# Performance work log

Hardware: AMD Instinct MI355X
Metric: run time of the kernel (lower is better)

## Reference

```python
import jax, jax.numpy as jnp
import numpy as np

T, H, I, E, K = 4096, 2048, 2816, 8, 2


def setup_inputs() -> dict:
    key = jax.random.key(0)
    k1, k2, k3, k4, k5 = jax.random.split(key, 5)
    x = jax.random.normal(k1, (T, H), dtype=jnp.float32)
    w13 = jax.random.normal(k2, (E, 2 * I, H), dtype=jnp.float32) * 0.02
    w2 = jax.random.normal(k3, (E, H, I), dtype=jnp.float32) * 0.02
    topk_weights = jax.random.uniform(k4, (T, K), dtype=jnp.float32)
    topk_ids = jax.random.randint(k5, (T, K), 0, E, dtype=jnp.int64)
    return {"x": x, "w13": w13, "w2": w2, "topk_weights": topk_weights, "topk_ids": topk_ids}


def reference(x, w13, w2, topk_weights, topk_ids):
    # SwiGLU MoE: per expert e, y_e = silu(x @ w1g_e^T) * (x @ w1u_e^T) @ w2_e^T
    # then combine with routing weights for the top-k selected experts.
    w_gate = w13[:, :I, :]   # [E, I, H]
    w_up = w13[:, I:, :]     # [E, I, H]
    gate = jnp.einsum('th,eih->eti', x, w_gate)  # [E, T, I]
    up = jnp.einsum('th,eih->eti', x, w_up)      # [E, T, I]
    act = jax.nn.silu(gate) * up                 # [E, T, I]
    y = jnp.einsum('eti,ehi->eth', act, w2)      # [E, T, H]
    # combine[t, e] = sum_k topk_weights[t, k] * (topk_ids[t, k] == e)
    onehot = (topk_ids[:, :, None] == jnp.arange(E)[None, None, :]).astype(x.dtype)  # [T, K, E]
    combine = jnp.einsum('tk,tke->te', topk_weights, onehot)  # [T, E]
    out = jnp.einsum('eth,te->th', y, combine)   # [T, H]
    return out
```

## Files before the change

### kernel.cpp

```cpp
#include <hip/hip_runtime.h>
#include <hip/hip_bf16.h>

#define TT 4096
#define HH 2048
#define CI 2816
#define EE 8
#define KK 2
#define TKN (TT * KK)
#define TM 128
#define BK 64
#define MAX_MT (TKN / TM + EE)
#define ROWS_PAD (MAX_MT * TM)

typedef short short8 __attribute__((ext_vector_type(8)));
typedef float floatx4 __attribute__((ext_vector_type(4)));

__device__ __forceinline__ unsigned short f2bf(float f) {
  unsigned u = __float_as_uint(f);
  return (unsigned short)((u + 0x8000u) >> 16);
}

__device__ __forceinline__ void cvt_store8(unsigned short* dst, float4 a, float4 b) {
  short8 v;
  v[0] = (short)f2bf(a.x); v[1] = (short)f2bf(a.y);
  v[2] = (short)f2bf(a.z); v[3] = (short)f2bf(a.w);
  v[4] = (short)f2bf(b.x); v[5] = (short)f2bf(b.y);
  v[6] = (short)f2bf(b.z); v[7] = (short)f2bf(b.w);
  *(short8*)dst = v;
}

__device__ __forceinline__ void gload_lds16(const unsigned short* g, unsigned short* l) {
  __builtin_amdgcn_global_load_lds(
      (const __attribute__((address_space(1))) unsigned int*)g,
      (__attribute__((address_space(3))) unsigned int*)l, 16, 0, 0);
}

__global__ void cvt_kernel(const float* __restrict__ src, unsigned short* __restrict__ dst,
                           int n8) {
  for (int i = blockIdx.x * blockDim.x + threadIdx.x; i < n8; i += gridDim.x * blockDim.x) {
    float4 a = ((const float4*)src)[2 * i];
    float4 b = ((const float4*)src)[2 * i + 1];
    cvt_store8(dst + (size_t)i * 8, a, b);
  }
}

__global__ void bucket_kernel(const int* __restrict__ ids, const float* __restrict__ tw,
                              int* __restrict__ hdr, int* __restrict__ tok,
                              float* __restrict__ wt) {
  __shared__ int cnt[EE];
  __shared__ int cur[EE];
  int tid = threadIdx.x;
  if (tid < EE) cnt[tid] = 0;
  __syncthreads();
  for (int p = tid; p < TKN; p += 256) atomicAdd(&cnt[ids[p]], 1);
  for (int r = tid; r < ROWS_PAD; r += 256) { tok[r] = 0; wt[r] = 0.f; }
  __syncthreads();
  if (tid == 0) {
    int rb = 0, tb = 0;
    for (int e = 0; e < EE; e++) {
      cur[e] = rb;
      int nt = (cnt[e] + TM - 1) / TM;
      for (int j = 0; j < nt; j++) hdr[1 + tb + j] = e;
      rb += nt * TM;
      tb += nt;
    }
    for (int m = tb; m < MAX_MT; m++) hdr[1 + m] = 0;
    hdr[0] = tb;
  }
  __syncthreads();
  for (int p = tid; p < TKN; p += 256) {
    int e = ids[p];
    int slot = atomicAdd(&cur[e], 1);
    tok[slot] = p / KK;
    wt[slot] = tw[p];
  }
}

__global__ __launch_bounds__(256, 2)
void gemm1_kernel(const unsigned short* __restrict__ xb, const unsigned short* __restrict__ w13b,
                  const int* __restrict__ hdr, const int* __restrict__ tok,
                  unsigned short* __restrict__ act) {
  const int mt = blockIdx.x;
  if (mt >= hdr[0]) return;
  const int e = hdr[1 + mt];
  const int bn = blockIdx.y;
  const int row_base = mt * TM;
  const int tid = threadIdx.x;
  const int lane = tid & 63;
  const int wave = tid >> 6;

  __shared__ __align__(16) unsigned short As[TM][BK];
  __shared__ __align__(16) unsigned short Bs[TM][BK];

  const int kcol = (lane & 7) * 8;
  const unsigned short* gA[4];
  const unsigned short* gB[4];
  unsigned short* lA[4];
  unsigned short* lB[4];
#pragma unroll
  for (int j = 0; j < 4; j++) {
    int r = wave * 32 + j * 8 + (lane >> 3);
    gA[j] = xb + (size_t)tok[row_base + r] * HH + kcol;
    int wrow = (r < 64) ? (bn * 64 + r) : (CI + bn * 64 + (r - 64));
    gB[j] = w13b + ((size_t)e * (2 * CI) + wrow) * HH + kcol;
    lA[j] = &As[wave * 32 + j * 8][0];
    lB[j] = &Bs[wave * 32 + j * 8][0];
  }

  floatx4 acc[2][8];
#pragma unroll
  for (int mi = 0; mi < 2; mi++)
#pragma unroll
    for (int ni = 0; ni < 8; ni++) acc[mi][ni] = (floatx4){0.f, 0.f, 0.f, 0.f};

  const int lrow = lane & 15;
  const int quad = lane >> 4;
  const int m0 = wave * 32;

  for (int k0 = 0; k0 < HH; k0 += BK) {
    __syncthreads();
#pragma unroll
    for (int j = 0; j < 4; j++) {
      gload_lds16(gA[j] + k0, lA[j]);
      gload_lds16(gB[j] + k0, lB[j]);
    }
    __syncthreads();
#pragma unroll
    for (int kh = 0; kh < 2; kh++) {
      short8 af0 = *(const short8*)&As[m0 + lrow][kh * 32 + quad * 8];
      short8 af1 = *(const short8*)&As[m0 + 16 + lrow][kh * 32 + quad * 8];
#pragma unroll
      for (int ni = 0; ni < 8; ni++) {
        short8 bf = *(const short8*)&Bs[ni * 16 + lrow][kh * 32 + quad * 8];
        acc[0][ni] = __builtin_amdgcn_mfma_f32_16x16x32_bf16(af0, bf, acc[0][ni], 0, 0, 0);
        acc[1][ni] = __builtin_amdgcn_mfma_f32_16x16x32_bf16(af1, bf, acc[1][ni], 0, 0, 0);
      }
    }
  }

  const int col0 = bn * 64;
#pragma unroll
  for (int mi = 0; mi < 2; mi++) {
#pragma unroll
    for (int ni = 0; ni < 4; ni++) {
#pragma unroll
      for (int r = 0; r < 4; r++) {
        float g = acc[mi][ni][r];
        float uu = acc[mi][ni + 4][r];
        float s = g / (1.f + __expf(-g));
        int row = row_base + m0 + mi * 16 + quad * 4 + r;
        int col = col0 + ni * 16 + lrow;
        act[(size_t)row * CI + col] = f2bf(s * uu);
      }
    }
  }
}

__global__ __launch_bounds__(256, 2)
void gemm2_kernel(const unsigned short* __restrict__ act, const unsigned short* __restrict__ w2b,
                  const int* __restrict__ hdr, const int* __restrict__ tok,
                  const float* __restrict__ wt, float* __restrict__ out) {
  const int mt = blockIdx.x;
  if (mt >= hdr[0]) return;
  const int e = hdr[1 + mt];
  const int h0 = blockIdx.y * TM;
  const int row_base = mt * TM;
  const int tid = threadIdx.x;
  const int lane = tid & 63;
  const int wave = tid >> 6;

  __shared__ __align__(16) unsigned short As[TM][BK];
  __shared__ __align__(16) unsigned short Bs[TM][BK];
  __shared__ int tok_s[TM];
  __shared__ float wt_s[TM];

  if (tid < TM) {
    tok_s[tid] = tok[row_base + tid];
    wt_s[tid] = wt[row_base + tid];
  }

  const int kcol = (lane & 7) * 8;
  const unsigned short* gA[4];
  const unsigned short* gB[4];
  unsigned short* lA[4];
  unsigned short* lB[4];
#pragma unroll
  for (int j = 0; j < 4; j++) {
    int r = wave * 32 + j * 8 + (lane >> 3);
    gA[j] = act + (size_t)(row_base + r) * CI + kcol;
    gB[j] = w2b + ((size_t)e * HH + h0 + r) * CI + kcol;
    lA[j] = &As[wave * 32 + j * 8][0];
    lB[j] = &Bs[wave * 32 + j * 8][0];
  }

  floatx4 acc[2][8];
#pragma unroll
  for (int mi = 0; mi < 2; mi++)
#pragma unroll
    for (int ni = 0; ni < 8; ni++) acc[mi][ni] = (floatx4){0.f, 0.f, 0.f, 0.f};

  const int lrow = lane & 15;
  const int quad = lane >> 4;
  const int m0 = wave * 32;

  for (int k0 = 0; k0 < CI; k0 += BK) {
    __syncthreads();
#pragma unroll
    for (int j = 0; j < 4; j++) {
      gload_lds16(gA[j] + k0, lA[j]);
      gload_lds16(gB[j] + k0, lB[j]);
    }
    __syncthreads();
#pragma unroll
    for (int kh = 0; kh < 2; kh++) {
      short8 af0 = *(const short8*)&As[m0 + lrow][kh * 32 + quad * 8];
      short8 af1 = *(const short8*)&As[m0 + 16 + lrow][kh * 32 + quad * 8];
#pragma unroll
      for (int ni = 0; ni < 8; ni++) {
        short8 bf = *(const short8*)&Bs[ni * 16 + lrow][kh * 32 + quad * 8];
        acc[0][ni] = __builtin_amdgcn_mfma_f32_16x16x32_bf16(af0, bf, acc[0][ni], 0, 0, 0);
        acc[1][ni] = __builtin_amdgcn_mfma_f32_16x16x32_bf16(af1, bf, acc[1][ni], 0, 0, 0);
      }
    }
  }

#pragma unroll
  for (int mi = 0; mi < 2; mi++) {
#pragma unroll
    for (int ni = 0; ni < 8; ni++) {
#pragma unroll
      for (int r = 0; r < 4; r++) {
        int lr = m0 + mi * 16 + quad * 4 + r;
        float w = wt_s[lr];
        if (w != 0.f) {
          atomicAdd(out + (size_t)tok_s[lr] * HH + h0 + ni * 16 + lrow, acc[mi][ni][r] * w);
        }
      }
    }
  }
}

extern "C" void kernel_launch(void* const* d_in, const int* in_sizes, int n_in,
                              void* d_out, int out_size, void* d_ws, size_t ws_size,
                              hipStream_t stream) {
  const float* x   = (const float*)d_in[0];
  const float* w13 = (const float*)d_in[1];
  const float* w2  = (const float*)d_in[2];
  const float* tw  = (const float*)d_in[3];
  const int*   ids = (const int*)d_in[4];
  float* out = (float*)d_out;

  char* ws = (char*)d_ws;
  int* hdr = (int*)ws;
  int* tok = (int*)(ws + 512);
  float* wt = (float*)(ws + 512 + ROWS_PAD * 4);
  unsigned short* act  = (unsigned short*)(ws + 74240);
  unsigned short* xb   = (unsigned short*)(ws + 74240 + 51904512ull);
  unsigned short* w13b = (unsigned short*)(ws + 74240 + 51904512ull + 16777216ull);
  unsigned short* w2b  = (unsigned short*)(ws + 74240 + 51904512ull + 16777216ull + 184549376ull);

  hipMemsetAsync(d_out, 0, (size_t)out_size * sizeof(float), stream);
  bucket_kernel<<<1, 256, 0, stream>>>(ids, tw, hdr, tok, wt);
  cvt_kernel<<<2048, 256, 0, stream>>>(x, xb, TT * HH / 8);
  cvt_kernel<<<4096, 256, 0, stream>>>(w13, w13b, EE * 2 * CI * HH / 8);
  cvt_kernel<<<4096, 256, 0, stream>>>(w2, w2b, EE * HH * CI / 8);
  gemm1_kernel<<<dim3(MAX_MT, CI / 64), 256, 0, stream>>>(xb, w13b, hdr, tok, act);
  gemm2_kernel<<<dim3(MAX_MT, HH / TM), 256, 0, stream>>>(act, w2b, hdr, tok, wt, out);
}
```

Before: 1.189 ms.

## Use 2x2 wave tiling and XOR-swizzled LDS layout in MoE GEMMs

Both grouped GEMM kernels switch from a 4x1 wave layout (32 rows x 128 cols per wave) to a 2x2 layout (64x64 per wave), which cuts LDS fragment reads per MFMA from 10 loads per 16 MFMAs to 8. The LDS tiles are XOR-swizzled on the 16-byte chunk index, both in the global-to-LDS load and in the fragment reads, to avoid bank conflicts on the 128-byte row stride. Launch bounds are raised to 4 blocks per CU, which limits register use and risks spills given the 64-register accumulator.

New measurement: 1.524 ms. 28.2% more time.

```diff
diff --git a/kernel.cpp b/kernel.cpp
--- a/kernel.cpp
+++ b/kernel.cpp
@@ -33,6 +33,10 @@
   __builtin_amdgcn_global_load_lds(
       (const __attribute__((address_space(1))) unsigned int*)g,
       (__attribute__((address_space(3))) unsigned int*)l, 16, 0, 0);
+}
+
+__device__ __forceinline__ short8 lds_frag(const unsigned short (*tile)[BK], int row, int chunk) {
+  return *(const short8*)&tile[row][((chunk ^ (row & 7)) << 3)];
 }
 
 __global__ void cvt_kernel(const float* __restrict__ src, unsigned short* __restrict__ dst,
@@ -76,7 +80,7 @@
   }
 }
 
-__global__ __launch_bounds__(256, 2)
+__global__ __launch_bounds__(256, 4)
 void gemm1_kernel(const unsigned short* __restrict__ xb, const unsigned short* __restrict__ w13b,
                   const int* __restrict__ hdr, const int* __restrict__ tok,
                   unsigned short* __restrict__ act) {
@@ -88,11 +92,13 @@
   const int tid = threadIdx.x;
   const int lane = tid & 63;
   const int wave = tid >> 6;
+  const int wr = wave & 1;
+  const int wc = wave >> 1;
 
   __shared__ __align__(16) unsigned short As[TM][BK];
   __shared__ __align__(16) unsigned short Bs[TM][BK];
 
-  const int kcol = (lane & 7) * 8;
+  const int kcol = (((lane & 7) ^ (lane >> 3)) * 8);
   const unsigned short* gA[4];
   const unsigned short* gB[4];
   unsigned short* lA[4];
@@ -107,15 +113,14 @@
     lB[j] = &Bs[wave * 32 + j * 8][0];
   }
 
-  floatx4 acc[2][8];
-#pragma unroll
-  for (int mi = 0; mi < 2; mi++)
-#pragma unroll
-    for (int ni = 0; ni < 8; ni++) acc[mi][ni] = (floatx4){0.f, 0.f, 0.f, 0.f};
+  floatx4 acc[4][4];
+#pragma unroll
+  for (int mi = 0; mi < 4; mi++)
+#pragma unroll
+    for (int ci = 0; ci < 4; ci++) acc[mi][ci] = (floatx4){0.f, 0.f, 0.f, 0.f};
 
   const int lrow = lane & 15;
   const int quad = lane >> 4;
-  const int m0 = wave * 32;
 
   for (int k0 = 0; k0 < HH; k0 += BK) {
     __syncthreads();
@@ -127,36 +132,40 @@
     __syncthreads();
 #pragma unroll
     for (int kh = 0; kh < 2; kh++) {
-      short8 af0 = *(const short8*)&As[m0 + lrow][kh * 32 + quad * 8];
-      short8 af1 = *(const short8*)&As[m0 + 16 + lrow][kh * 32 + quad * 8];
-#pragma unroll
-      for (int ni = 0; ni < 8; ni++) {
-        short8 bf = *(const short8*)&Bs[ni * 16 + lrow][kh * 32 + quad * 8];
-        acc[0][ni] = __builtin_amdgcn_mfma_f32_16x16x32_bf16(af0, bf, acc[0][ni], 0, 0, 0);
-        acc[1][ni] = __builtin_amdgcn_mfma_f32_16x16x32_bf16(af1, bf, acc[1][ni], 0, 0, 0);
-      }
-    }
-  }
-
-  const int col0 = bn * 64;
-#pragma unroll
-  for (int mi = 0; mi < 2; mi++) {
-#pragma unroll
-    for (int ni = 0; ni < 4; ni++) {
+      const int chunk = kh * 4 + quad;
+      short8 a[4], b[4];
+#pragma unroll
+      for (int mi = 0; mi < 4; mi++) a[mi] = lds_frag(As, wr * 64 + mi * 16 + lrow, chunk);
+      b[0] = lds_frag(Bs, wc * 32 + lrow, chunk);
+      b[1] = lds_frag(Bs, wc * 32 + 16 + lrow, chunk);
+      b[2] = lds_frag(Bs, 64 + wc * 32 + lrow, chunk);
+      b[3] = lds_frag(Bs, 64 + wc * 32 + 16 + lrow, chunk);
+#pragma unroll
+      for (int mi = 0; mi < 4; mi++)
+#pragma unroll
+        for (int ci = 0; ci < 4; ci++)
+          acc[mi][ci] = __builtin_amdgcn_mfma_f32_16x16x32_bf16(a[mi], b[ci], acc[mi][ci], 0, 0, 0);
+    }
+  }
+
+#pragma unroll
+  for (int mi = 0; mi < 4; mi++) {
+#pragma unroll
+    for (int cg = 0; cg < 2; cg++) {
 #pragma unroll
       for (int r = 0; r < 4; r++) {
-        float g = acc[mi][ni][r];
-        float uu = acc[mi][ni + 4][r];
+        float g = acc[mi][cg][r];
+        float uu = acc[mi][cg + 2][r];
         float s = g / (1.f + __expf(-g));
-        int row = row_base + m0 + mi * 16 + quad * 4 + r;
-        int col = col0 + ni * 16 + lrow;
+        int row = row_base + wr * 64 + mi * 16 + quad * 4 + r;
+        int col = bn * 64 + wc * 32 + cg * 16 + lrow;
         act[(size_t)row * CI + col] = f2bf(s * uu);
       }
     }
   }
 }
 
-__global__ __launch_bounds__(256, 2)
+__global__ __launch_bounds__(256, 4)
 void gemm2_kernel(const unsigned short* __restrict__ act, const unsigned short* __restrict__ w2b,
                   const int* __restrict__ hdr, const int* __restrict__ tok,
                   const float* __restrict__ wt, float* __restrict__ out) {
@@ -168,6 +177,8 @@
   const int tid = threadIdx.x;
   const int lane = tid & 63;
   const int wave = tid >> 6;
+  const int wr = wave & 1;
+  const int wc = wave >> 1;
 
   __shared__ __align__(16) unsigned short As[TM][BK];
   __shared__ __align__(16) unsigned short Bs[TM][BK];
@@ -179,7 +190,7 @@
     wt_s[tid] = wt[row_base + tid];
   }
 
-  const int kcol = (lane & 7) * 8;
+  const int kcol = (((lane & 7) ^ (lane >> 3)) * 8);
   const unsigned short* gA[4];
   const unsigned short* gB[4];
   unsigned short* lA[4];
@@ -193,15 +204,14 @@
     lB[j] = &Bs[wave * 32 + j * 8][0];
   }
 
-  floatx4 acc[2][8];
-#pragma unroll
-  for (int mi = 0; mi < 2; mi++)
-#pragma unroll
-    for (int ni = 0; ni < 8; ni++) acc[mi][ni] = (floatx4){0.f, 0.f, 0.f, 0.f};
+  floatx4 acc[4][4];
+#pragma unroll
+  for (int mi = 0; mi < 4; mi++)
+#pragma unroll
+    for (int ci = 0; ci < 4; ci++) acc[mi][ci] = (floatx4){0.f, 0.f, 0.f, 0.f};
 
   const int lrow = lane & 15;
   const int quad = lane >> 4;
-  const int m0 = wave * 32;
 
   for (int k0 = 0; k0 < CI; k0 += BK) {
     __syncthreads();
@@ -213,27 +223,31 @@
     __syncthreads();
 #pragma unroll
     for (int kh = 0; kh < 2; kh++) {
-      short8 af0 = *(const short8*)&As[m0 + lrow][kh * 32 + quad * 8];
-      short8 af1 = *(const short8*)&As[m0 + 16 + lrow][kh * 32 + quad * 8];
-#pragma unroll
-      for (int ni = 0; ni < 8; ni++) {
-        short8 bf = *(const short8*)&Bs[ni * 16 + lrow][kh * 32 + quad * 8];
-        acc[0][ni] = __builtin_amdgcn_mfma_f32_16x16x32_bf16(af0, bf, acc[0][ni], 0, 0, 0);
-        acc[1][ni] = __builtin_amdgcn_mfma_f32_16x16x32_bf16(af1, bf, acc[1][ni], 0, 0, 0);
-      }
-    }
-  }
-
-#pragma unroll
-  for (int mi = 0; mi < 2; mi++) {
-#pragma unroll
-    for (int ni = 0; ni < 8; ni++) {
+      const int chunk = kh * 4 + quad;
+      short8 a[4], b[4];
+#pragma unroll
+      for (int mi = 0; mi < 4; mi++) a[mi] = lds_frag(As, wr * 64 + mi * 16 + lrow, chunk);
+#pragma unroll
+      for (int ci = 0; ci < 4; ci++) b[ci] = lds_frag(Bs, wc * 64 + ci * 16 + lrow, chunk);
+#pragma unroll
+      for (int mi = 0; mi < 4; mi++)
+#pragma unroll
+        for (int ci = 0; ci < 4; ci++)
+          acc[mi][ci] = __builtin_amdgcn_mfma_f32_16x16x32_bf16(a[mi], b[ci], acc[mi][ci], 0, 0, 0);
+    }
+  }
+
+#pragma unroll
+  for (int mi = 0; mi < 4; mi++) {
+#pragma unroll
+    for (int ci = 0; ci < 4; ci++) {
 #pragma unroll
       for (int r = 0; r < 4; r++) {
-        int lr = m0 + mi * 16 + quad * 4 + r;
+        int lr = wr * 64 + mi * 16 + quad * 4 + r;
         float w = wt_s[lr];
         if (w != 0.f) {
-          atomicAdd(out + (size_t)tok_s[lr] * HH + h0 + ni * 16 + lrow, acc[mi][ni][r] * w);
+          atomicAdd(out + (size_t)tok_s[lr] * HH + h0 + wc * 64 + ci * 16 + lrow,
+                    acc[mi][ci][r] * w);
         }
       }
     }
```
